# Kernel tuning notes

Measured on AMD Instinct MI355X. Metric: run time of the kernel, lower is better.

The kernel has to match this reference:

```python
import jax, jax.numpy as jnp
import numpy as np

N_NODES = 100000
N_EDGES = 3200000
IN_F = 128
HID = 128


def setup_inputs() -> dict:
    key = jax.random.key(0)
    ks = jax.random.split(key, 6)
    features = jax.random.normal(ks[0], (N_NODES, IN_F), dtype=jnp.float32)
    edge_index = jax.random.randint(ks[1], (2, N_EDGES), 0, N_NODES, dtype=jnp.int64)
    # Glorot-ish scaled weights
    W1 = jax.random.normal(ks[2], (IN_F, HID), dtype=jnp.float32) / np.sqrt(IN_F)
    b1 = jnp.zeros((HID,), dtype=jnp.float32)
    W2 = jax.random.normal(ks[3], (HID, HID), dtype=jnp.float32) / np.sqrt(HID)
    b2 = jnp.zeros((HID,), dtype=jnp.float32)
    prelu_a = jnp.full((HID,), 0.25, dtype=jnp.float32)  # nn.PReLU default init
    return {"features": features, "edge_index": edge_index,
            "W1": W1, "b1": b1, "W2": W2, "b2": b2, "prelu_a": prelu_a}


def _prelu(x, a):
    return jnp.where(x >= 0, x, a[None, :] * x)


def _graph_conv(x, W, b, a, src, dst, dout_is, din_is):
    # DGL GraphConv, norm='both': src-normalize, SpMM aggregate, dst-normalize,
    # dense transform, bias, activation.
    h = x * dout_is[:, None]                                   # [N, F]
    m = jax.ops.segment_sum(h[src], dst, num_segments=N_NODES)  # gather + scatter-add
    m = m * din_is[:, None]
    m = m @ W + b[None, :]
    return _prelu(m, a)


def reference(features, edge_index, W1, b1, W2, b2, prelu_a):
    src, dst = edge_index[0], edge_index[1]
    ones = jnp.ones((N_EDGES,), dtype=jnp.float32)
    deg_out = jax.ops.segment_sum(ones, src, num_segments=N_NODES)
    deg_in = jax.ops.segment_sum(ones, dst, num_segments=N_NODES)
    dout_is = jax.lax.rsqrt(jnp.clip(deg_out, 1.0))
    din_is = jax.lax.rsqrt(jnp.clip(deg_in, 1.0))
    h = _graph_conv(features, W1, b1, prelu_a, src, dst, dout_is, din_is)
    h = _graph_conv(h, W2, b2, prelu_a, src, dst, dout_is, din_is)
    return h
```

## Files before the change

### kernel.cpp

```cpp
#include <hip/hip_runtime.h>
#include <hip/hip_fp16.h>

#define NN 100000
#define EE 3200000
#define FF 128

#define NBUK 391
#define CAP 12288
#define CH_A 8192
#define NB_A ((EE + CH_A - 1) / CH_A)
#define NCH 8

typedef _Float16 f16x8 __attribute__((ext_vector_type(8)));
typedef float f32x4 __attribute__((ext_vector_type(4)));

__global__ __launch_bounds__(256) void k_bin(const int* __restrict__ ei,
                                             int* __restrict__ dcur_g,
                                             int* __restrict__ scur_g,
                                             int2* __restrict__ binned,
                                             int* __restrict__ src_binned) {
  __shared__ int hd[NBUK];
  __shared__ int hs[NBUK];
  __shared__ int cd[NBUK];
  __shared__ int cs[NBUK];
  int tid = threadIdx.x;
  for (int t = tid; t < NBUK; t += 256) { hd[t] = 0; hs[t] = 0; }
  __syncthreads();
  int base = blockIdx.x * CH_A;
  const int* dst = ei + EE;
#pragma unroll
  for (int k = 0; k < CH_A / 256; ++k) {
    int e = base + k * 256 + tid;
    if (e < EE) {
      atomicAdd(&hs[ei[e] >> 8], 1);
      atomicAdd(&hd[dst[e] >> 8], 1);
    }
  }
  __syncthreads();
  for (int t = tid; t < NBUK; t += 256) {
    cd[t] = (hd[t] > 0) ? atomicAdd(&dcur_g[t], hd[t]) : 0;
    cs[t] = (hs[t] > 0) ? atomicAdd(&scur_g[t], hs[t]) : 0;
  }
  __syncthreads();
#pragma unroll
  for (int k = 0; k < CH_A / 256; ++k) {
    int e = base + k * 256 + tid;
    if (e < EE) {
      int s = ei[e];
      int d = dst[e];
      int db = d >> 8;
      int dpos = atomicAdd(&cd[db], 1);
      binned[(size_t)db * CAP + dpos] = make_int2(s, d);
      int sb = s >> 8;
      int spos = atomicAdd(&cs[sb], 1);
      src_binned[(size_t)sb * CAP + spos] = s;
    }
  }
}

__global__ __launch_bounds__(256) void k_csr(const int2* __restrict__ binned,
                                             const int* __restrict__ dcnt,
                                             int2* __restrict__ offs2,
                                             float* __restrict__ din_is,
                                             int* __restrict__ csr_src) {
  __shared__ int h2[256 * NCH];
  __shared__ int sa[256];
  __shared__ int cur2[256 * NCH];
  int tid = threadIdx.x;
  int b = blockIdx.x;
  int dst0 = b << 8;
  int gbeg = b * CAP;
  int cnt = dcnt[b];

#pragma unroll
  for (int i = 0; i < NCH; ++i) h2[tid * NCH + i] = 0;
  __syncthreads();
  for (int t = tid; t < cnt; t += 256) {
    int2 p = binned[gbeg + t];
    int c = (unsigned)p.x / 12500u;
    atomicAdd(&h2[(p.y - dst0) * NCH + c], 1);
  }
  __syncthreads();
  int deg = 0;
#pragma unroll
  for (int i = 0; i < NCH; ++i) deg += h2[tid * NCH + i];
  sa[tid] = deg;
  __syncthreads();
  for (int off = 1; off < 256; off <<= 1) {
    int v = (tid >= off) ? sa[tid - off] : 0;
    __syncthreads();
    sa[tid] += v;
    __syncthreads();
  }
  int excl = sa[tid] - deg;
  int run = gbeg + excl;
#pragma unroll
  for (int i = 0; i < NCH; ++i) { cur2[tid * NCH + i] = run; run += h2[tid * NCH + i]; }
  int node = dst0 + tid;
  if (node < NN) {
    offs2[node] = make_int2(gbeg + excl, gbeg + excl + deg);
    int d = deg < 1 ? 1 : deg;
    din_is[node] = rsqrtf((float)d);
  }
  __syncthreads();
  for (int t = tid; t < cnt; t += 256) {
    int2 p = binned[gbeg + t];
    int c = (unsigned)p.x / 12500u;
    int pos = atomicAdd(&cur2[(p.y - dst0) * NCH + c], 1);
    csr_src[pos] = p.x;
  }
}

__global__ __launch_bounds__(256) void k_srchist(const int* __restrict__ src_binned,
                                                 const int* __restrict__ scnt,
                                                 float* __restrict__ dout_is) {
  __shared__ int h[256];
  int tid = threadIdx.x;
  int b = blockIdx.x;
  int src0 = b << 8;
  int gbeg = b * CAP;
  int cnt = scnt[b];
  h[tid] = 0;
  __syncthreads();
  for (int t = tid; t < cnt; t += 256) {
    atomicAdd(&h[src_binned[gbeg + t] - src0], 1);
  }
  __syncthreads();
  int node = src0 + tid;
  if (node < NN) {
    int d = h[tid]; if (d < 1) d = 1;
    dout_is[node] = rsqrtf((float)d);
  }
}

__global__ __launch_bounds__(256) void k_wprep(const float* __restrict__ W,
                                               __half* __restrict__ Wt) {
  int t = blockIdx.x * blockDim.x + threadIdx.x;
  if (t >= FF * FF) return;
  int n = t >> 7, k = t & 127;
  Wt[n * FF + k] = __float2half(W[k * FF + n]);
}

__global__ __launch_bounds__(256) void k_prescale_h(const float* __restrict__ x,
                                                    const float* __restrict__ dout_is,
                                                    __half* __restrict__ xh) {
  int t = blockIdx.x * blockDim.x + threadIdx.x;
  if (t >= NN * (FF / 4)) return;
  int node = t >> 5;
  float sc = dout_is[node];
  float4 v = ((const float4*)x)[t];
  union { __half2 h[2]; uint2 u; } p;
  p.h[0] = __floats2half2_rn(v.x * sc, v.y * sc);
  p.h[1] = __floats2half2_rn(v.z * sc, v.w * sc);
  ((uint2*)xh)[t] = p.u;
}

__global__ __launch_bounds__(256) void k_agg(const __half* __restrict__ xh,
                                             const float* __restrict__ din_is,
                                             const int2* __restrict__ offs2,
                                             const int* __restrict__ csr_src,
                                             __half* __restrict__ outh) {
  int gid = blockIdx.x * blockDim.x + threadIdx.x;
  int node = gid >> 6;
  int lane = threadIdx.x & 63;
  if (node >= NN) return;
  int2 oo = offs2[node];
  int beg = oo.x, end = oo.y;
  float ax = 0.f, ay = 0.f, bx = 0.f, by = 0.f;
  int e = beg;
  for (; e < end && (e & 3); ++e) {
    int s = csr_src[e];
    float2 v = __half22float2(((const __half2*)(xh + (size_t)s * FF))[lane]);
    ax += v.x; ay += v.y;
  }
  for (; e + 8 <= end; e += 8) {
    int4 i0 = *(const int4*)(csr_src + e);
    int4 i1 = *(const int4*)(csr_src + e + 4);
    float2 v0 = __half22float2(((const __half2*)(xh + (size_t)i0.x * FF))[lane]);
    float2 v1 = __half22float2(((const __half2*)(xh + (size_t)i0.y * FF))[lane]);
    float2 v2 = __half22float2(((const __half2*)(xh + (size_t)i0.z * FF))[lane]);
    float2 v3 = __half22float2(((const __half2*)(xh + (size_t)i0.w * FF))[lane]);
    float2 v4 = __half22float2(((const __half2*)(xh + (size_t)i1.x * FF))[lane]);
    float2 v5 = __half22float2(((const __half2*)(xh + (size_t)i1.y * FF))[lane]);
    float2 v6 = __half22float2(((const __half2*)(xh + (size_t)i1.z * FF))[lane]);
    float2 v7 = __half22float2(((const __half2*)(xh + (size_t)i1.w * FF))[lane]);
    ax += v0.x; ay += v0.y; bx += v1.x; by += v1.y;
    ax += v2.x; ay += v2.y; bx += v3.x; by += v3.y;
    ax += v4.x; ay += v4.y; bx += v5.x; by += v5.y;
    ax += v6.x; ay += v6.y; bx += v7.x; by += v7.y;
  }
  for (; e < end; ++e) {
    int s = csr_src[e];
    float2 v = __half22float2(((const __half2*)(xh + (size_t)s * FF))[lane]);
    ax += v.x; ay += v.y;
  }
  float di = din_is[node];
  __half2 r = __floats2half2_rn((ax + bx) * di, (ay + by) * di);
  ((__half2*)(outh + (size_t)node * FF))[lane] = r;
}

__global__ __launch_bounds__(256) void k_gemm_mfma(const __half* __restrict__ X,
                                                   const __half* __restrict__ Wt,
                                                   const float* __restrict__ bias,
                                                   const float* __restrict__ pa,
                                                   const float* __restrict__ postscale,
                                                   int out_half,
                                                   float* __restrict__ outf,
                                                   __half* __restrict__ outh) {
  __shared__ __half Xs[64][FF + 8];
  __shared__ __half Ws[FF][FF + 8];
  int tid = threadIdx.x;
  int row0 = blockIdx.x * 64;

  for (int t = tid; t < 64 * 16; t += 256) {
    int r = t >> 4, c8 = (t & 15) * 8;
    int row = row0 + r;
    uint4 v = make_uint4(0, 0, 0, 0);
    if (row < NN) v = *(const uint4*)(X + (size_t)row * FF + c8);
    *(uint4*)&Xs[r][c8] = v;
  }
  for (int t = tid; t < FF * 16; t += 256) {
    int r = t >> 4, c8 = (t & 15) * 8;
    uint4 v = *(const uint4*)(Wt + r * FF + c8);
    *(uint4*)&Ws[r][c8] = v;
  }
  __syncthreads();

  int wid = tid >> 6;
  int lane = tid & 63;
  int l15 = lane & 15;
  int g = lane >> 4;
  int arow = wid * 16 + l15;

  f32x4 acc[8];
#pragma unroll
  for (int n = 0; n < 8; ++n) acc[n] = (f32x4){0.f, 0.f, 0.f, 0.f};

  union FU { uint2 u[2]; f16x8 v; };
#pragma unroll
  for (int kk = 0; kk < 4; ++kk) {
    int kb = kk * 32;
    FU a;
    a.u[0] = *(const uint2*)&Xs[arow][kb + 4 * g];
    a.u[1] = *(const uint2*)&Xs[arow][kb + 16 + 4 * g];
#pragma unroll
    for (int n = 0; n < 8; ++n) {
      FU b;
      int wr = n * 16 + l15;
      b.u[0] = *(const uint2*)&Ws[wr][kb + 4 * g];
      b.u[1] = *(const uint2*)&Ws[wr][kb + 16 + 4 * g];
      acc[n] = __builtin_amdgcn_mfma_f32_16x16x32_f16(a.v, b.v, acc[n], 0, 0, 0);
    }
  }

#pragma unroll
  for (int n = 0; n < 8; ++n) {
    int col = n * 16 + l15;
    float bb = bias[col];
    float aa = pa[col];
#pragma unroll
    for (int j = 0; j < 4; ++j) {
      int row = row0 + wid * 16 + g * 4 + j;
      if (row < NN) {
        float v = acc[n][j] + bb;
        v = v >= 0.f ? v : aa * v;
        if (out_half) {
          v *= postscale[row];
          outh[(size_t)row * FF + col] = __float2half(v);
        } else {
          outf[(size_t)row * FF + col] = v;
        }
      }
    }
  }
}

extern "C" void kernel_launch(void* const* d_in, const int* in_sizes, int n_in,
                              void* d_out, int out_size, void* d_ws, size_t ws_size,
                              hipStream_t stream) {
  const float* features = (const float*)d_in[0];
  const int*   ei       = (const int*)d_in[1];
  const float* W1       = (const float*)d_in[2];
  const float* b1       = (const float*)d_in[3];
  const float* W2       = (const float*)d_in[4];
  const float* b2       = (const float*)d_in[5];
  const float* pa       = (const float*)d_in[6];
  float* out = (float*)d_out;

  char* ws = (char*)d_ws;
  size_t off = 0;
  auto alloc = [&](size_t bytes) -> void* {
    void* p = ws + off;
    off += (bytes + 255) & ~(size_t)255;
    return p;
  };
  int*    cur     = (int*)alloc((size_t)2 * NBUK * 4);
  int*    dcur    = cur;
  int*    scur    = cur + NBUK;
  float*  dout_is = (float*)alloc((size_t)NN * 4);
  float*  din_is  = (float*)alloc((size_t)NN * 4);
  int2*   offs2   = (int2*)alloc((size_t)NN * 8);
  int*    csr_src = (int*)alloc((size_t)NBUK * CAP * 4);
  int2*   binned  = (int2*)alloc((size_t)NBUK * CAP * 8);
  int*    src_binned = (int*)alloc((size_t)NBUK * CAP * 4);
  __half* tmp_h   = (__half*)alloc((size_t)NN * FF * 2);
  __half* w1t     = (__half*)alloc((size_t)FF * FF * 2);
  __half* w2t     = (__half*)alloc((size_t)FF * FF * 2);
  __half* xh      = (__half*)binned;

  (void)hipMemsetAsync(cur, 0, (size_t)2 * NBUK * 4, stream);

  k_bin<<<NB_A, 256, 0, stream>>>(ei, dcur, scur, binned, src_binned);
  k_csr<<<NBUK, 256, 0, stream>>>(binned, dcur, offs2, din_is, csr_src);
  k_srchist<<<NBUK, 256, 0, stream>>>(src_binned, scur, dout_is);

  k_wprep<<<(FF * FF + 255) / 256, 256, 0, stream>>>(W1, w1t);
  k_wprep<<<(FF * FF + 255) / 256, 256, 0, stream>>>(W2, w2t);

  k_prescale_h<<<(NN * FF / 4 + 255) / 256, 256, 0, stream>>>(features, dout_is, xh);
  k_agg<<<NN / 4, 256, 0, stream>>>(xh, din_is, offs2, csr_src, tmp_h);
  k_gemm_mfma<<<(NN + 63) / 64, 256, 0, stream>>>(tmp_h, w1t, b1, pa, dout_is, 1, nullptr, xh);

  k_agg<<<NN / 4, 256, 0, stream>>>(xh, din_is, offs2, csr_src, tmp_h);
  k_gemm_mfma<<<(NN + 63) / 64, 256, 0, stream>>>(tmp_h, w2t, b2, pa, nullptr, 0, out, nullptr);
}
```

Measured before the change: 450.3 us.

## Pack binned edges into 32-bit records, stage in LDS, widen aggregation unroll

Each binned edge is now stored as one 32-bit word, the local destination in the top 8 bits and the source in the low 24, instead of an int2 pair. This halves binned traffic. k_csr copies a bucket's records into LDS once and builds the CSR from a plain per-destination histogram. It drops the 8-way source-range sub-sorting, which kept neighbours roughly grouped by source for gather locality. The aggregation loop now gathers 16 edges per iteration into four accumulator pairs, with a 4-edge tail loop, and the index and feature loads in prescale use nontemporal hints. The risks are worse gather locality in k_agg, lower k_csr occupancy from about 48KB of LDS per block, and xh now spilling past the smaller binned buffer into src_binned.

```diff
diff --git a/kernel.cpp b/kernel.cpp
--- a/kernel.cpp
+++ b/kernel.cpp
@@ -9,15 +9,16 @@
 #define CAP 12288
 #define CH_A 8192
 #define NB_A ((EE + CH_A - 1) / CH_A)
-#define NCH 8
 
 typedef _Float16 f16x8 __attribute__((ext_vector_type(8)));
 typedef float f32x4 __attribute__((ext_vector_type(4)));
+typedef int vint4 __attribute__((ext_vector_type(4)));
+typedef float vfloat4 __attribute__((ext_vector_type(4)));
 
 __global__ __launch_bounds__(256) void k_bin(const int* __restrict__ ei,
                                              int* __restrict__ dcur_g,
                                              int* __restrict__ scur_g,
-                                             int2* __restrict__ binned,
+                                             unsigned int* __restrict__ binned,
                                              int* __restrict__ src_binned) {
   __shared__ int hd[NBUK];
   __shared__ int hs[NBUK];
@@ -50,7 +51,7 @@
       int d = dst[e];
       int db = d >> 8;
       int dpos = atomicAdd(&cd[db], 1);
-      binned[(size_t)db * CAP + dpos] = make_int2(s, d);
+      binned[(size_t)db * CAP + dpos] = ((unsigned int)(d & 255) << 24) | (unsigned int)s;
       int sb = s >> 8;
       int spos = atomicAdd(&cs[sb], 1);
       src_binned[(size_t)sb * CAP + spos] = s;
@@ -58,33 +59,26 @@
   }
 }
 
-__global__ __launch_bounds__(256) void k_csr(const int2* __restrict__ binned,
+__global__ __launch_bounds__(256) void k_csr(const unsigned int* __restrict__ binned,
                                              const int* __restrict__ dcnt,
                                              int2* __restrict__ offs2,
                                              float* __restrict__ din_is,
                                              int* __restrict__ csr_src) {
-  __shared__ int h2[256 * NCH];
+  __shared__ unsigned int recs[CAP];
+  __shared__ int h[256];
   __shared__ int sa[256];
-  __shared__ int cur2[256 * NCH];
+  __shared__ int cur[256];
   int tid = threadIdx.x;
   int b = blockIdx.x;
-  int dst0 = b << 8;
   int gbeg = b * CAP;
   int cnt = dcnt[b];
 
-#pragma unroll
-  for (int i = 0; i < NCH; ++i) h2[tid * NCH + i] = 0;
-  __syncthreads();
-  for (int t = tid; t < cnt; t += 256) {
-    int2 p = binned[gbeg + t];
-    int c = (unsigned)p.x / 12500u;
-    atomicAdd(&h2[(p.y - dst0) * NCH + c], 1);
-  }
-  __syncthreads();
-  int deg = 0;
-#pragma unroll
-  for (int i = 0; i < NCH; ++i) deg += h2[tid * NCH + i];
-  sa[tid] = deg;
+  for (int t = tid; t < cnt; t += 256) recs[t] = binned[gbeg + t];
+  h[tid] = 0;
+  __syncthreads();
+  for (int t = tid; t < cnt; t += 256) atomicAdd(&h[recs[t] >> 24], 1);
+  __syncthreads();
+  sa[tid] = h[tid];
   __syncthreads();
   for (int off = 1; off < 256; off <<= 1) {
     int v = (tid >= off) ? sa[tid - off] : 0;
@@ -92,11 +86,10 @@
     sa[tid] += v;
     __syncthreads();
   }
+  int deg = h[tid];
   int excl = sa[tid] - deg;
-  int run = gbeg + excl;
-#pragma unroll
-  for (int i = 0; i < NCH; ++i) { cur2[tid * NCH + i] = run; run += h2[tid * NCH + i]; }
-  int node = dst0 + tid;
+  cur[tid] = gbeg + excl;
+  int node = (b << 8) + tid;
   if (node < NN) {
     offs2[node] = make_int2(gbeg + excl, gbeg + excl + deg);
     int d = deg < 1 ? 1 : deg;
@@ -104,10 +97,9 @@
   }
   __syncthreads();
   for (int t = tid; t < cnt; t += 256) {
-    int2 p = binned[gbeg + t];
-    int c = (unsigned)p.x / 12500u;
-    int pos = atomicAdd(&cur2[(p.y - dst0) * NCH + c], 1);
-    csr_src[pos] = p.x;
+    unsigned int r = recs[t];
+    int pos = atomicAdd(&cur[r >> 24], 1);
+    csr_src[pos] = (int)(r & 0xFFFFFFu);
   }
 }
 
@@ -148,7 +140,7 @@
   if (t >= NN * (FF / 4)) return;
   int node = t >> 5;
   float sc = dout_is[node];
-  float4 v = ((const float4*)x)[t];
+  vfloat4 v = __builtin_nontemporal_load((const vfloat4*)x + t);
   union { __half2 h[2]; uint2 u; } p;
   p.h[0] = __floats2half2_rn(v.x * sc, v.y * sc);
   p.h[1] = __floats2half2_rn(v.z * sc, v.w * sc);
@@ -167,15 +159,18 @@
   int2 oo = offs2[node];
   int beg = oo.x, end = oo.y;
   float ax = 0.f, ay = 0.f, bx = 0.f, by = 0.f;
+  float cx = 0.f, cy = 0.f, dx = 0.f, dy = 0.f;
   int e = beg;
   for (; e < end && (e & 3); ++e) {
     int s = csr_src[e];
     float2 v = __half22float2(((const __half2*)(xh + (size_t)s * FF))[lane]);
     ax += v.x; ay += v.y;
   }
-  for (; e + 8 <= end; e += 8) {
-    int4 i0 = *(const int4*)(csr_src + e);
-    int4 i1 = *(const int4*)(csr_src + e + 4);
+  for (; e + 16 <= end; e += 16) {
+    vint4 i0 = __builtin_nontemporal_load((const vint4*)(csr_src + e));
+    vint4 i1 = __builtin_nontemporal_load((const vint4*)(csr_src + e + 4));
+    vint4 i2 = __builtin_nontemporal_load((const vint4*)(csr_src + e + 8));
+    vint4 i3 = __builtin_nontemporal_load((const vint4*)(csr_src + e + 12));
     float2 v0 = __half22float2(((const __half2*)(xh + (size_t)i0.x * FF))[lane]);
     float2 v1 = __half22float2(((const __half2*)(xh + (size_t)i0.y * FF))[lane]);
     float2 v2 = __half22float2(((const __half2*)(xh + (size_t)i0.z * FF))[lane]);
@@ -184,10 +179,31 @@
     float2 v5 = __half22float2(((const __half2*)(xh + (size_t)i1.y * FF))[lane]);
     float2 v6 = __half22float2(((const __half2*)(xh + (size_t)i1.z * FF))[lane]);
     float2 v7 = __half22float2(((const __half2*)(xh + (size_t)i1.w * FF))[lane]);
+    float2 v8 = __half22float2(((const __half2*)(xh + (size_t)i2.x * FF))[lane]);
+    float2 v9 = __half22float2(((const __half2*)(xh + (size_t)i2.y * FF))[lane]);
+    float2 va = __half22float2(((const __half2*)(xh + (size_t)i2.z * FF))[lane]);
+    float2 vb = __half22float2(((const __half2*)(xh + (size_t)i2.w * FF))[lane]);
+    float2 vc = __half22float2(((const __half2*)(xh + (size_t)i3.x * FF))[lane]);
+    float2 vd = __half22float2(((const __half2*)(xh + (size_t)i3.y * FF))[lane]);
+    float2 ve = __half22float2(((const __half2*)(xh + (size_t)i3.z * FF))[lane]);
+    float2 vf = __half22float2(((const __half2*)(xh + (size_t)i3.w * FF))[lane]);
     ax += v0.x; ay += v0.y; bx += v1.x; by += v1.y;
-    ax += v2.x; ay += v2.y; bx += v3.x; by += v3.y;
+    cx += v2.x; cy += v2.y; dx += v3.x; dy += v3.y;
     ax += v4.x; ay += v4.y; bx += v5.x; by += v5.y;
-    ax += v6.x; ay += v6.y; bx += v7.x; by += v7.y;
+    cx += v6.x; cy += v6.y; dx += v7.x; dy += v7.y;
+    ax += v8.x; ay += v8.y; bx += v9.x; by += v9.y;
+    cx += va.x; cy += va.y; dx += vb.x; dy += vb.y;
+    ax += vc.x; ay += vc.y; bx += vd.x; by += vd.y;
+    cx += ve.x; cy += ve.y; dx += vf.x; dy += vf.y;
+  }
+  for (; e + 4 <= end; e += 4) {
+    vint4 i0 = __builtin_nontemporal_load((const vint4*)(csr_src + e));
+    float2 v0 = __half22float2(((const __half2*)(xh + (size_t)i0.x * FF))[lane]);
+    float2 v1 = __half22float2(((const __half2*)(xh + (size_t)i0.y * FF))[lane]);
+    float2 v2 = __half22float2(((const __half2*)(xh + (size_t)i0.z * FF))[lane]);
+    float2 v3 = __half22float2(((const __half2*)(xh + (size_t)i0.w * FF))[lane]);
+    ax += v0.x; ay += v0.y; bx += v1.x; by += v1.y;
+    cx += v2.x; cy += v2.y; dx += v3.x; dy += v3.y;
   }
   for (; e < end; ++e) {
     int s = csr_src[e];
@@ -195,7 +211,7 @@
     ax += v.x; ay += v.y;
   }
   float di = din_is[node];
-  __half2 r = __floats2half2_rn((ax + bx) * di, (ay + by) * di);
+  __half2 r = __floats2half2_rn((ax + bx + cx + dx) * di, (ay + by + cy + dy) * di);
   ((__half2*)(outh + (size_t)node * FF))[lane] = r;
 }
 
@@ -301,8 +317,8 @@
   float*  din_is  = (float*)alloc((size_t)NN * 4);
   int2*   offs2   = (int2*)alloc((size_t)NN * 8);
   int*    csr_src = (int*)alloc((size_t)NBUK * CAP * 4);
-  int2*   binned  = (int2*)alloc((size_t)NBUK * CAP * 8);
-  int*    src_binned = (int*)alloc((size_t)NBUK * CAP * 4);
+  unsigned int* binned = (unsigned int*)alloc((size_t)NBUK * CAP * 4);
+  int*    src_binned   = (int*)alloc((size_t)NBUK * CAP * 4);
   __half* tmp_h   = (__half*)alloc((size_t)NN * FF * 2);
   __half* w1t     = (__half*)alloc((size_t)FF * FF * 2);
   __half* w2t     = (__half*)alloc((size_t)FF * FF * 2);
```

New measurement: 446.3 us. No clear change (-0.9%).
